# Kernel optimization log

Hardware: AMD Instinct MI355X
Metric: run time of the kernel (lower is better)

## Reference

```python
import jax, jax.numpy as jnp
import numpy as np

H = 128  # hidden_dim


def gcn_conv(x, src, dst, n, W, b):
    """PyG GCNConv: add self-loops, symmetric norm, gather-transform-scatter."""
    h = x @ W  # [n, H]
    loop = jnp.arange(n, dtype=src.dtype)
    s = jnp.concatenate([src, loop])
    d = jnp.concatenate([dst, loop])
    deg = jax.ops.segment_sum(jnp.ones(s.shape[0], h.dtype), d, num_segments=n)
    dinv = jnp.where(deg > 0, jax.lax.rsqrt(deg), 0.0)
    norm = dinv[s] * dinv[d]  # [E+n]
    msg = h[s] * norm[:, None]
    out = jax.ops.segment_sum(msg, d, num_segments=n)
    return out + b


def encode(x, edge_index, batch, num_graphs, params):
    src, dst = edge_index[0], edge_index[1]
    n = x.shape[0]
    for (W, b) in params:
        x = jax.nn.relu(gcn_conv(x, src, dst, n, W, b))
    sums = jax.ops.segment_sum(x, batch, num_segments=num_graphs)
    cnts = jax.ops.segment_sum(jnp.ones((n, 1), x.dtype), batch, num_segments=num_graphs)
    return sums / jnp.maximum(cnts, 1.0)  # global_mean_pool -> [B, H]


def setup_inputs() -> dict:
    key = jax.random.key(0)
    ks = jax.random.split(key, 32)
    B, C = 32, 5
    Nd, Ed = 1280, 5120
    Np, Ep = 12800, 204800
    f32 = jnp.float32

    def lin(k, fan_in, fan_out):
        k1, k2 = jax.random.split(k)
        lim = 1.0 / np.sqrt(fan_in)
        W = jax.random.uniform(k1, (fan_in, fan_out), f32, -lim, lim)
        b = jax.random.uniform(k2, (fan_out,), f32, -lim, lim)
        return W, b

    Wd0, bd0 = lin(ks[0], 78, H)
    Wd1, bd1 = lin(ks[1], H, H)
    Wd2, bd2 = lin(ks[2], H, H)
    Wp0, bp0 = lin(ks[3], 1280, H)
    Wp1, bp1 = lin(ks[4], H, H)
    Wp2, bp2 = lin(ks[5], H, H)
    Wq, bq = lin(ks[6], H, H)
    Wk, bk = lin(ks[7], H, H)
    Wv, bv = lin(ks[8], H, H)
    W1, b1 = lin(ks[9], 2 * H, H)
    W2, b2 = lin(ks[10], H, 1)

    drug_x = jax.random.normal(ks[11], (Nd, 78), f32)
    prot_x = jax.random.normal(ks[12], (C, Np, 1280), f32)
    drug_edge_index = jax.random.randint(ks[13], (2, Ed), 0, Nd, jnp.int32)
    prot_edge_index = jax.random.randint(ks[14], (C, 2, Ep), 0, Np, jnp.int32)
    # equal-sized graphs per batch element -> every segment non-empty
    drug_batch = (jnp.arange(Nd, dtype=jnp.int32) * B) // Nd
    prot_batch = (jnp.arange(Np, dtype=jnp.int32) * B) // Np

    return dict(drug_x=drug_x, prot_x=prot_x,
                Wd0=Wd0, bd0=bd0, Wd1=Wd1, bd1=bd1, Wd2=Wd2, bd2=bd2,
                Wp0=Wp0, bp0=bp0, Wp1=Wp1, bp1=bp1, Wp2=Wp2, bp2=bp2,
                Wq=Wq, bq=bq, Wk=Wk, bk=bk, Wv=Wv, bv=bv,
                W1=W1, b1=b1, W2=W2, b2=b2,
                drug_edge_index=drug_edge_index, prot_edge_index=prot_edge_index,
                drug_batch=drug_batch, prot_batch=prot_batch, num_graphs=B)


def reference(drug_x, prot_x, Wd0, bd0, Wd1, bd1, Wd2, bd2,
              Wp0, bp0, Wp1, bp1, Wp2, bp2,
              Wq, bq, Wk, bk, Wv, bv, W1, b1, W2, b2,
              drug_edge_index, prot_edge_index, drug_batch, prot_batch, num_graphs):
    drug_params = [(Wd0, bd0), (Wd1, bd1), (Wd2, bd2)]
    prot_params = [(Wp0, bp0), (Wp1, bp1), (Wp2, bp2)]

    drug_emb = encode(drug_x, drug_edge_index, drug_batch, num_graphs, drug_params)  # [B,H]

    # vmap over conformations -> [C, B, H]
    conf = jax.vmap(lambda x, ei: encode(x, ei, prot_batch, num_graphs, prot_params))(
        prot_x, prot_edge_index)
    conf = jnp.transpose(conf, (1, 0, 2))  # [B, C, H]

    # drug-conditioned cross-attention over conformations
    q = drug_emb @ Wq + bq                      # [B,H]
    keys = conf @ Wk + bk                       # [B,C,H]
    vals = conf @ Wv + bv                       # [B,C,H]
    scores = jnp.einsum('bh,bch->bc', q, keys) / jnp.sqrt(jnp.asarray(H, q.dtype))
    attn = jax.nn.softmax(scores, axis=1)       # [B,C]
    protein_emb = jnp.einsum('bc,bch->bh', attn, vals)

    combined = jnp.concatenate([drug_emb, protein_emb], axis=1)  # [B,2H]
    hidden = jax.nn.relu(combined @ W1 + b1)    # dropout is identity in eval mode
    logits = (hidden @ W2 + b2)[:, 0]           # [B]
    return logits, attn
```

## Files before the change

### kernel.cpp

```cpp
#include <hip/hip_runtime.h>

#define H     128
#define BGR   32
#define NCONF 5
#define ND    1280
#define FD    78
#define ED    5120
#define NP    12800
#define FP    1280
#define EP    204800
#define MAXD  64

#define PROT_GEMM_BLKS 500
#define DRUG_GEMM1_BLKS 20
#define DRUG_GEMM_BLKS 10
#define PLACE_BLKS 4020
#define PROT_MP_BLKS 16000
#define DRUG_MP_BLKS 320

typedef unsigned short u16;
typedef unsigned int   u32;
typedef __attribute__((ext_vector_type(8))) short bf16x8;
typedef __attribute__((ext_vector_type(4))) unsigned int u32x4;
typedef __attribute__((ext_vector_type(4))) unsigned short u16x4;
typedef __attribute__((ext_vector_type(8))) unsigned short u16x8;
typedef __attribute__((ext_vector_type(4))) float f32x4;

__device__ __forceinline__ u16 f2bf(float x) {
  u32 u = __float_as_uint(x);
  u32 r = (u + 0x7FFFu + ((u >> 16) & 1u)) >> 16;
  return (u16)r;
}
__device__ __forceinline__ float bf2f(u16 h) {
  return __uint_as_float(((u32)h) << 16);
}

__device__ __forceinline__ void gload16(const void* gsrc, void* lds) {
  __builtin_amdgcn_global_load_lds(
      (const __attribute__((address_space(1))) unsigned int*)gsrc,
      (__attribute__((address_space(3))) unsigned int*)lds, 16, 0, 0);
}

__device__ __forceinline__ void cvt8(float4 p, float4 q, bf16x8& hi, bf16x8& lo) {
  float f[8] = {p.x, p.y, p.z, p.w, q.x, q.y, q.z, q.w};
  u32x4 h, l;
  #pragma unroll
  for (int j = 0; j < 4; ++j) {
    u32 u0 = __float_as_uint(f[2 * j]);
    u32 u1 = __float_as_uint(f[2 * j + 1]);
    u32 h0 = u0 & 0xFFFF0000u;
    u32 h1 = u1 & 0xFFFF0000u;
    h[j] = (h0 >> 16) | h1;
    float l0 = f[2 * j]     - __uint_as_float(h0);
    float l1 = f[2 * j + 1] - __uint_as_float(h1);
    l[j] = (__float_as_uint(l0) >> 16) | (__float_as_uint(l1) & 0xFFFF0000u);
  }
  union { u32x4 u; bf16x8 b; } ch, cl;
  ch.u = h; cl.u = l;
  hi = ch.b; lo = cl.b;
}

__device__ __forceinline__ void splitW_chunk(
    const float* __restrict__ W, u16* __restrict__ wsW, int K, int g)
{
  int step = g >> 10;
  int r = g & 1023;
  int col = r >> 3, q = r & 7;
  int u = q ^ (col & 7);
  int kc = (u & 3) * 8;
  bool lo = u >= 4;
  int k0 = step * 32 + kc;
  u16x8 o;
  #pragma unroll
  for (int j = 0; j < 8; ++j) {
    float x = W[(size_t)(k0 + j) * 128 + col];
    u16 h = f2bf(x);
    o[j] = lo ? f2bf(x - bf2f(h)) : h;
  }
  *(u16x8*)(wsW + (size_t)g * 8) = o;
}

__global__ __launch_bounds__(256) void splitW_all_k(
    const float* __restrict__ Wp0, const float* __restrict__ Wp1,
    const float* __restrict__ Wp2, const float* __restrict__ Wd1,
    const float* __restrict__ Wd2,
    u16* __restrict__ o0, u16* __restrict__ o1, u16* __restrict__ o2,
    u16* __restrict__ o3, u16* __restrict__ o4)
{
  int g = blockIdx.x * 256 + threadIdx.x;
  if      (g < 40960) splitW_chunk(Wp0, o0, FP, g);
  else if (g < 45056) splitW_chunk(Wp1, o1, H, g - 40960);
  else if (g < 49152) splitW_chunk(Wp2, o2, H, g - 45056);
  else if (g < 53248) splitW_chunk(Wd1, o3, H, g - 49152);
  else if (g < 57344) splitW_chunk(Wd2, o4, H, g - 53248);
}

__device__ __forceinline__ void gemm_pipe_body(
    char* smemRaw, const float* __restrict__ A, const u16* __restrict__ wsW,
    u16* __restrict__ Cout, int K, int blk)
{
  u16* Wlds = (u16*)smemRaw;
  const int t = threadIdx.x;
  const int wid = t >> 6, lane = t & 63;
  const int lane15 = lane & 15, lq = lane >> 4;
  const int m0 = blk * 128;
  const int NT = K >> 5;

  const float* Ar0 = A + (size_t)(m0 + wid * 32 + lane15) * K + lq * 8;
  const float* Ar1 = Ar0 + (size_t)16 * K;
  const u16* sbase = wsW + (size_t)(wid * 4) * 512 + (size_t)lane * 8;

  f32x4 acc[2][8];
  #pragma unroll
  for (int i = 0; i < 2; ++i)
    #pragma unroll
    for (int j = 0; j < 8; ++j)
      acc[i][j] = (f32x4){0.f, 0.f, 0.f, 0.f};

  #define STAGE_W(step, buf) do {                                   \
    const u16* s_ = sbase + (size_t)(step) * 8192;                  \
    u16* d_ = &Wlds[(buf) * 8192 + wid * 2048];                     \
    gload16(s_,        d_);                                         \
    gload16(s_ + 512,  d_ + 512);                                   \
    gload16(s_ + 1024, d_ + 1024);                                  \
    gload16(s_ + 1536, d_ + 1536);                                  \
  } while (0)

  STAGE_W(0, 0);
  asm volatile("" ::: "memory");
  float4 xa0 = *(const float4*)(Ar0);
  float4 xa1 = *(const float4*)(Ar0 + 4);
  float4 xb0 = *(const float4*)(Ar1);
  float4 xb1 = *(const float4*)(Ar1 + 4);
  asm volatile("" ::: "memory");
  float4 ya0 = *(const float4*)(Ar0 + 32);
  float4 ya1 = *(const float4*)(Ar0 + 36);
  float4 yb0 = *(const float4*)(Ar1 + 32);
  float4 yb1 = *(const float4*)(Ar1 + 36);

  #define BODY(T, RA0, RA1, RB0, RB1) do {                                    \
    if ((T) < NT - 1) asm volatile("s_waitcnt vmcnt(4)\ns_barrier" ::: "memory"); \
    else              asm volatile("s_waitcnt vmcnt(0)\ns_barrier"  ::: "memory"); \
    if ((T) + 1 < NT) { STAGE_W((T) + 1, ((T) + 1) & 1); }                    \
    asm volatile("" ::: "memory");                                            \
    bf16x8 ah0, al0, ah1, al1;                                                \
    cvt8(RA0, RA1, ah0, al0);                                                 \
    cvt8(RB0, RB1, ah1, al1);                                                 \
    if ((T) + 2 < NT) {                                                       \
      const float* p0_ = Ar0 + (size_t)((T) + 2) * 32;                        \
      const float* p1_ = Ar1 + (size_t)((T) + 2) * 32;                        \
      RA0 = *(const float4*)(p0_); RA1 = *(const float4*)(p0_ + 4);           \
      RB0 = *(const float4*)(p1_); RB1 = *(const float4*)(p1_ + 4);           \
    }                                                                         \
    const char* base_ = (const char*)&Wlds[((T) & 1) * 8192];                 \
    _Pragma("unroll")                                                         \
    for (int cb = 0; cb < 8; ++cb) {                                          \
      int col_ = cb * 16 + lane15;                                            \
      const char* cbp_ = base_ + col_ * 128;                                  \
      int sw_ = (col_ & 7) << 4;                                              \
      bf16x8 bh_ = *(const bf16x8*)(cbp_ + ((lq << 4) ^ sw_));                \
      bf16x8 bl_ = *(const bf16x8*)(cbp_ + (((lq | 4) << 4) ^ sw_));          \
      acc[0][cb] = __builtin_amdgcn_mfma_f32_16x16x32_bf16(ah0, bh_, acc[0][cb], 0, 0, 0); \
      acc[0][cb] = __builtin_amdgcn_mfma_f32_16x16x32_bf16(al0, bh_, acc[0][cb], 0, 0, 0); \
      acc[0][cb] = __builtin_amdgcn_mfma_f32_16x16x32_bf16(ah0, bl_, acc[0][cb], 0, 0, 0); \
      acc[1][cb] = __builtin_amdgcn_mfma_f32_16x16x32_bf16(ah1, bh_, acc[1][cb], 0, 0, 0); \
      acc[1][cb] = __builtin_amdgcn_mfma_f32_16x16x32_bf16(al1, bh_, acc[1][cb], 0, 0, 0); \
      acc[1][cb] = __builtin_amdgcn_mfma_f32_16x16x32_bf16(ah1, bl_, acc[1][cb], 0, 0, 0); \
    }                                                                         \
  } while (0)

  for (int tt = 0; tt < NT; tt += 2) {
    BODY(tt,     xa0, xa1, xb0, xb1);
    BODY(tt + 1, ya0, ya1, yb0, yb1);
  }
  #undef BODY
  #undef STAGE_W

  #pragma unroll
  for (int rb = 0; rb < 2; ++rb) {
    #pragma unroll
    for (int j = 0; j < 4; ++j) {
      int row = m0 + wid * 32 + rb * 16 + lq * 4 + j;
      u16* Crow = Cout + (size_t)row * 128 + lane15;
      #pragma unroll
      for (int cb = 0; cb < 8; ++cb)
        Crow[cb * 16] = f2bf(acc[rb][cb][j]);
    }
  }
}

__device__ __forceinline__ void gemm_f32_body(
    char* smemRaw, const float* __restrict__ A, const float* __restrict__ W,
    u16* __restrict__ Cout, int K, int blk)
{
  float* As = (float*)smemRaw;
  float* Bs = (float*)(smemRaw + 16 * 64 * 4);
  const int t = threadIdx.x;
  const int m0 = blk * 64;
  const int colg = (t & 31) * 4;
  const int rowg = (t >> 5) * 8;
  const int rA = t >> 2;
  const int cA = (t & 3) * 4;
  const int rB = t >> 4;
  const int cB = (t & 15) * 4;

  float acc[8][4] = {};

  for (int k0 = 0; k0 < K; k0 += 16) {
    __syncthreads();
    #pragma unroll
    for (int j = 0; j < 4; ++j) {
      int kk = k0 + cA + j;
      As[(cA + j) * 64 + rA] = (kk < K) ? A[(size_t)(m0 + rA) * K + kk] : 0.0f;
    }
    {
      int kk = k0 + rB;
      if (kk < K) {
        *(float4*)&Bs[rB * 128 + cB]      = *(const float4*)(W + (size_t)kk * 128 + cB);
        *(float4*)&Bs[rB * 128 + cB + 64] = *(const float4*)(W + (size_t)kk * 128 + cB + 64);
      } else {
        *(float4*)&Bs[rB * 128 + cB]      = make_float4(0.f, 0.f, 0.f, 0.f);
        *(float4*)&Bs[rB * 128 + cB + 64] = make_float4(0.f, 0.f, 0.f, 0.f);
      }
    }
    __syncthreads();
    #pragma unroll
    for (int k = 0; k < 16; ++k) {
      float4 b  = *(const float4*)&Bs[k * 128 + colg];
      float4 a0 = *(const float4*)&As[k * 64 + rowg];
      float4 a1 = *(const float4*)&As[k * 64 + rowg + 4];
      const float av[8] = {a0.x, a0.y, a0.z, a0.w, a1.x, a1.y, a1.z, a1.w};
      #pragma unroll
      for (int i = 0; i < 8; ++i) {
        acc[i][0] += av[i] * b.x;
        acc[i][1] += av[i] * b.y;
        acc[i][2] += av[i] * b.z;
        acc[i][3] += av[i] * b.w;
      }
    }
  }
  #pragma unroll
  for (int i = 0; i < 8; ++i) {
    u16x4 o;
    o[0] = f2bf(acc[i][0]); o[1] = f2bf(acc[i][1]);
    o[2] = f2bf(acc[i][2]); o[3] = f2bf(acc[i][3]);
    *(u16x4*)(Cout + (size_t)(m0 + rowg + i) * 128 + colg) = o;
  }
}

__global__ __launch_bounds__(256, 4) void stage1_place_k(
    const float* __restrict__ pA, const u16* __restrict__ pW, u16* __restrict__ pC,
    const float* __restrict__ dA, const float* __restrict__ dW, u16* __restrict__ dC,
    const int* __restrict__ prot_ei, const int* __restrict__ drug_ei,
    int* __restrict__ deg_p, u16* __restrict__ slot_p,
    int* __restrict__ deg_d, u16* __restrict__ slot_d)
{
  __shared__ __align__(16) char smem[2 * 16384];
  int b = blockIdx.x;
  if (b < PROT_GEMM_BLKS) {
    gemm_pipe_body(smem, pA, pW, pC, FP, b);
    return;
  }
  b -= PROT_GEMM_BLKS;
  if (b < DRUG_GEMM1_BLKS) {
    gemm_f32_body(smem, dA, dW, dC, FD, b);
    return;
  }
  b -= DRUG_GEMM1_BLKS;
  int idx = b * 256 + threadIdx.x;
  if (idx < NCONF * EP) {
    int c = idx / EP, e = idx - c * EP;
    const int* eic = prot_ei + (size_t)c * 2 * EP;
    int s = eic[e], d = eic[EP + e];
    int node = c * NP + d;
    int pos = atomicAdd(&deg_p[node], 1);
    if (pos < MAXD) slot_p[(size_t)node * MAXD + pos] = (u16)s;
  } else {
    idx -= NCONF * EP;
    if (idx < ED) {
      int s = drug_ei[idx], d = drug_ei[ED + idx];
      int pos = atomicAdd(&deg_d[d], 1);
      if (pos < MAXD) slot_d[(size_t)d * MAXD + pos] = (u16)s;
    }
  }
}

__global__ __launch_bounds__(256, 4) void stage23_gemm_k(
    const float* __restrict__ pA, const u16* __restrict__ pW, u16* __restrict__ pC,
    const float* __restrict__ dA, const u16* __restrict__ dW, u16* __restrict__ dC)
{
  __shared__ __align__(16) char smem[2 * 16384];
  if (blockIdx.x < PROT_GEMM_BLKS)
    gemm_pipe_body(smem, pA, pW, pC, H, blockIdx.x);
  else
    gemm_pipe_body(smem, dA, dW, dC, H, blockIdx.x - PROT_GEMM_BLKS);
}

__device__ __forceinline__ void mp_body(
    const u16* __restrict__ h, float* __restrict__ xout,
    const int* __restrict__ deg, const u16* __restrict__ slots,
    const float* __restrict__ bias, int wid, int nPer)
{
  int lane = threadIdx.x & 63;
  int c = wid / nPer;
  const int* dg = deg + (size_t)c * nPer;
  int v = wid - c * nPer;
  const u32* hc = (const u32*)(h + (size_t)c * nPer * H);
  const u16* sl = slots + (size_t)wid * MAXD;
  int degv = dg[v];
  float dv = rsqrtf((float)degv + 1.0f);
  u32 us = ((const u32*)h)[(size_t)wid * 64 + lane];
  float a0x = __uint_as_float(us << 16) * dv;
  float a0y = __uint_as_float(us & 0xFFFF0000u) * dv;
  float a1x = 0.f, a1y = 0.f;
  int n = degv < MAXD ? degv : MAXD;
  int i = 0;
  for (; i + 4 <= n; i += 4) {
    int s0 = sl[i], s1 = sl[i + 1], s2 = sl[i + 2], s3 = sl[i + 3];
    float d0 = rsqrtf((float)dg[s0] + 1.0f);
    float d1 = rsqrtf((float)dg[s1] + 1.0f);
    float d2 = rsqrtf((float)dg[s2] + 1.0f);
    float d3 = rsqrtf((float)dg[s3] + 1.0f);
    u32 u0 = hc[(size_t)s0 * 64 + lane];
    u32 u1 = hc[(size_t)s1 * 64 + lane];
    u32 u2 = hc[(size_t)s2 * 64 + lane];
    u32 u3 = hc[(size_t)s3 * 64 + lane];
    a0x += __uint_as_float(u0 << 16) * d0;
    a0y += __uint_as_float(u0 & 0xFFFF0000u) * d0;
    a1x += __uint_as_float(u1 << 16) * d1;
    a1y += __uint_as_float(u1 & 0xFFFF0000u) * d1;
    a0x += __uint_as_float(u2 << 16) * d2;
    a0y += __uint_as_float(u2 & 0xFFFF0000u) * d2;
    a1x += __uint_as_float(u3 << 16) * d3;
    a1y += __uint_as_float(u3 & 0xFFFF0000u) * d3;
  }
  for (; i < n; ++i) {
    int s0 = sl[i];
    float d0 = rsqrtf((float)dg[s0] + 1.0f);
    u32 u0 = hc[(size_t)s0 * 64 + lane];
    a0x += __uint_as_float(u0 << 16) * d0;
    a0y += __uint_as_float(u0 & 0xFFFF0000u) * d0;
  }
  int col = lane * 2;
  float ox = fmaxf((a0x + a1x) * dv + bias[col],     0.0f);
  float oy = fmaxf((a0y + a1y) * dv + bias[col + 1], 0.0f);
  ((float2*)(xout + (size_t)wid * H))[lane] = make_float2(ox, oy);
}

__global__ __launch_bounds__(256) void mp_all_k(
    const u16* __restrict__ hp, float* __restrict__ xp,
    const int* __restrict__ degp, const u16* __restrict__ slotp,
    const float* __restrict__ biasp,
    const u16* __restrict__ hd, float* __restrict__ xd,
    const int* __restrict__ degd, const u16* __restrict__ slotd,
    const float* __restrict__ biasd)
{
  int blk = blockIdx.x;
  int wv = threadIdx.x >> 6;
  if (blk < PROT_MP_BLKS) {
    mp_body(hp, xp, degp, slotp, biasp, blk * 4 + wv, NP);
  } else {
    mp_body(hd, xd, degd, slotd, biasd, (blk - PROT_MP_BLKS) * 4 + wv, ND);
  }
}

__device__ __forceinline__ void pool_body(
    const float* __restrict__ x, float* __restrict__ out, int blk, int npg)
{
  __shared__ float part[4][128];
  const int col = threadIdx.x & 127;
  const int rp  = threadIdx.x >> 7;
  size_t row0 = (size_t)blk * npg;
  float acc = 0.0f;
  for (int i = rp; i < npg; i += 4)
    acc += x[(row0 + i) * H + col];
  part[rp][col] = acc;
  __syncthreads();
  if (rp == 0)
    out[(size_t)blk * H + col] =
        (part[0][col] + part[1][col] + part[2][col] + part[3][col]) / (float)npg;
}

__global__ __launch_bounds__(512) void pool_all_k(
    const float* __restrict__ xd, float* __restrict__ outd,
    const float* __restrict__ xp, float* __restrict__ outp)
{
  if (blockIdx.x < BGR) pool_body(xd, outd, blockIdx.x, ND / BGR);
  else                  pool_body(xp, outp, blockIdx.x - BGR, NP / BGR);
}

__global__ __launch_bounds__(128) void attn_mlp_k(
    const float* __restrict__ drug_emb, const float* __restrict__ conf_pool,
    const float* __restrict__ Wq, const float* __restrict__ bq,
    const float* __restrict__ Wk, const float* __restrict__ bk,
    const float* __restrict__ Wv, const float* __restrict__ bv,
    const float* __restrict__ W1, const float* __restrict__ b1,
    const float* __restrict__ W2, const float* __restrict__ b2,
    float* __restrict__ out)
{
  const int b = blockIdx.x;
  const int hcol = threadIdx.x;
  __shared__ float de[H], pc[H], vals_s[NCONF][H], red[H], sc[NCONF], peS[H];

  de[hcol] = drug_emb[(size_t)b * H + hcol];
  __syncthreads();

  float qv = bq[hcol];
  for (int k = 0; k < H; ++k) qv += de[k] * Wq[k * H + hcol];

  for (int c = 0; c < NCONF; ++c) {
    __syncthreads();
    pc[hcol] = conf_pool[((size_t)c * BGR + b) * H + hcol];
    __syncthreads();
    float kk = bk[hcol], vv = bv[hcol];
    for (int k = 0; k < H; ++k) {
      float p = pc[k];
      kk += p * Wk[k * H + hcol];
      vv += p * Wv[k * H + hcol];
    }
    vals_s[c][hcol] = vv;
    red[hcol] = qv * kk;
    __syncthreads();
    for (int s = 64; s > 0; s >>= 1) {
      if (hcol < s) red[hcol] += red[hcol + s];
      __syncthreads();
    }
    if (hcol == 0) sc[c] = red[0] * 0.08838834764831845f;
  }
  __syncthreads();

  float m = sc[0];
  for (int c = 1; c < NCONF; ++c) m = fmaxf(m, sc[c]);
  float ex[NCONF], sum = 0.0f;
  for (int c = 0; c < NCONF; ++c) { ex[c] = expf(sc[c] - m); sum += ex[c]; }
  float inv = 1.0f / sum;
  if (hcol < NCONF) out[BGR + b * NCONF + hcol] = ex[hcol] * inv;

  float pe = 0.0f;
  for (int c = 0; c < NCONF; ++c) pe += (ex[c] * inv) * vals_s[c][hcol];
  peS[hcol] = pe;
  __syncthreads();

  float hid = b1[hcol];
  for (int k = 0; k < H; ++k) hid += de[k]  * W1[k * H + hcol];
  for (int k = 0; k < H; ++k) hid += peS[k] * W1[(H + k) * H + hcol];
  hid = fmaxf(hid, 0.0f);

  red[hcol] = hid * W2[hcol];
  __syncthreads();
  for (int s = 64; s > 0; s >>= 1) {
    if (hcol < s) red[hcol] += red[hcol + s];
    __syncthreads();
  }
  if (hcol == 0) out[b] = red[0] + b2[0];
}

extern "C" void kernel_launch(void* const* d_in, const int* in_sizes, int n_in,
                              void* d_out, int out_size, void* d_ws, size_t ws_size,
                              hipStream_t stream)
{
  const float* drug_x  = (const float*)d_in[0];
  const float* prot_x  = (const float*)d_in[1];
  const float* Wd0 = (const float*)d_in[2];  const float* bd0 = (const float*)d_in[3];
  const float* Wd1 = (const float*)d_in[4];  const float* bd1 = (const float*)d_in[5];
  const float* Wd2 = (const float*)d_in[6];  const float* bd2 = (const float*)d_in[7];
  const float* Wp0 = (const float*)d_in[8];  const float* bp0 = (const float*)d_in[9];
  const float* Wp1 = (const float*)d_in[10]; const float* bp1 = (const float*)d_in[11];
  const float* Wp2 = (const float*)d_in[12]; const float* bp2 = (const float*)d_in[13];
  const float* Wq  = (const float*)d_in[14]; const float* bq  = (const float*)d_in[15];
  const float* Wk  = (const float*)d_in[16]; const float* bk  = (const float*)d_in[17];
  const float* Wv  = (const float*)d_in[18]; const float* bv  = (const float*)d_in[19];
  const float* W1  = (const float*)d_in[20]; const float* b1  = (const float*)d_in[21];
  const float* W2  = (const float*)d_in[22]; const float* b2  = (const float*)d_in[23];
  const int* drug_ei = (const int*)d_in[24];
  const int* prot_ei = (const int*)d_in[25];
  float* out = (float*)d_out;

  char* base = (char*)d_ws;
  size_t off = 0;
  auto alloc = [&](size_t bytes) -> char* {
    char* p = base + off;
    off = (off + bytes + 255) & ~(size_t)255;
    return p;
  };
  int*   deg_p   = (int*)  alloc((size_t)NCONF * NP * 4);
  int*   deg_d   = (int*)  alloc((size_t)ND * 4);
  const size_t ctrBytes = (size_t)NCONF * NP * 4 + (size_t)ND * 4;

  u16*   slot_p  = (u16*)  alloc((size_t)NCONF * NP * MAXD * 2);
  u16*   slot_d  = (u16*)  alloc((size_t)ND * MAXD * 2);
  u16*   bufHp   = (u16*)  alloc((size_t)NCONF * NP * H * 2);
  float* bufXp   = (float*)alloc((size_t)NCONF * NP * H * 4);
  u16*   bufHd   = (u16*)  alloc((size_t)ND * H * 2);
  float* bufXd   = (float*)alloc((size_t)ND * H * 4);
  float* drugemb = (float*)alloc((size_t)BGR * H * 4);
  float* confp   = (float*)alloc((size_t)NCONF * BGR * H * 4);
  u16* Wp0ws = (u16*)alloc((size_t)FP * 512);
  u16* Wp1ws = (u16*)alloc((size_t)H * 512);
  u16* Wp2ws = (u16*)alloc((size_t)H * 512);
  u16* Wd1ws = (u16*)alloc((size_t)H * 512);
  u16* Wd2ws = (u16*)alloc((size_t)H * 512);

  hipMemsetAsync(deg_p, 0, ctrBytes, stream);

  splitW_all_k<<<224, 256, 0, stream>>>(Wp0, Wp1, Wp2, Wd1, Wd2,
                                        Wp0ws, Wp1ws, Wp2ws, Wd1ws, Wd2ws);

  stage1_place_k<<<PROT_GEMM_BLKS + DRUG_GEMM1_BLKS + PLACE_BLKS, 256, 0, stream>>>(
      prot_x, Wp0ws, bufHp, drug_x, Wd0, bufHd,
      prot_ei, drug_ei, deg_p, slot_p, deg_d, slot_d);

  mp_all_k<<<PROT_MP_BLKS + DRUG_MP_BLKS, 256, 0, stream>>>(
      bufHp, bufXp, deg_p, slot_p, bp0,
      bufHd, bufXd, deg_d, slot_d, bd0);
  stage23_gemm_k<<<PROT_GEMM_BLKS + DRUG_GEMM_BLKS, 256, 0, stream>>>(
      bufXp, Wp1ws, bufHp, bufXd, Wd1ws, bufHd);
  mp_all_k<<<PROT_MP_BLKS + DRUG_MP_BLKS, 256, 0, stream>>>(
      bufHp, bufXp, deg_p, slot_p, bp1,
      bufHd, bufXd, deg_d, slot_d, bd1);
  stage23_gemm_k<<<PROT_GEMM_BLKS + DRUG_GEMM_BLKS, 256, 0, stream>>>(
      bufXp, Wp2ws, bufHp, bufXd, Wd2ws, bufHd);
  mp_all_k<<<PROT_MP_BLKS + DRUG_MP_BLKS, 256, 0, stream>>>(
      bufHp, bufXp, deg_p, slot_p, bp2,
      bufHd, bufXd, deg_d, slot_d, bd2);

  pool_all_k<<<BGR + NCONF * BGR, 512, 0, stream>>>(bufXd, drugemb, bufXp, confp);

  attn_mlp_k<<<BGR, 128, 0, stream>>>(drugemb, confp, Wq, bq, Wk, bk, Wv, bv,
                                      W1, b1, W2, b2, out);
}
```

Measured before the change: 410.9 us.

## Store layer activations in bf16 and feed GEMM with bf16 A directly

The message-passing output buffers change from fp32 to bf16, which halves their write traffic, the A-operand reads in the layer 2/3 GEMMs and the pool reads. A new GEMM body loads bf16 A rows directly into MFMA operands instead of converting fp32. The degree-counter memset is folded into the weight-split kernel, removing one API call. In exchange, the activations lose precision: the old path split each value into hi and lo bf16 parts, and now there is a single bf16 rounding, which may affect accuracy.

```diff
diff --git a/kernel.cpp b/kernel.cpp
--- a/kernel.cpp
+++ b/kernel.cpp
@@ -85,9 +85,14 @@
     const float* __restrict__ Wp2, const float* __restrict__ Wd1,
     const float* __restrict__ Wd2,
     u16* __restrict__ o0, u16* __restrict__ o1, u16* __restrict__ o2,
-    u16* __restrict__ o3, u16* __restrict__ o4)
+    u16* __restrict__ o3, u16* __restrict__ o4,
+    int* __restrict__ deg_p, int* __restrict__ deg_d)
 {
   int g = blockIdx.x * 256 + threadIdx.x;
+  for (int i = g; i < NCONF * NP + ND; i += 224 * 256) {
+    if (i < NCONF * NP) deg_p[i] = 0;
+    else                deg_d[i - NCONF * NP] = 0;
+  }
   if      (g < 40960) splitW_chunk(Wp0, o0, FP, g);
   else if (g < 45056) splitW_chunk(Wp1, o1, H, g - 40960);
   else if (g < 49152) splitW_chunk(Wp2, o2, H, g - 45056);
@@ -189,6 +194,92 @@
   }
 }
 
+__device__ __forceinline__ void gemm_pipe_bf16A_body(
+    char* smemRaw, const u16* __restrict__ A, const u16* __restrict__ wsW,
+    u16* __restrict__ Cout, int K, int blk)
+{
+  u16* Wlds = (u16*)smemRaw;
+  const int t = threadIdx.x;
+  const int wid = t >> 6, lane = t & 63;
+  const int lane15 = lane & 15, lq = lane >> 4;
+  const int m0 = blk * 128;
+  const int NT = K >> 5;
+
+  const u16* Ar0 = A + (size_t)(m0 + wid * 32 + lane15) * K + lq * 8;
+  const u16* Ar1 = Ar0 + (size_t)16 * K;
+  const u16* sbase = wsW + (size_t)(wid * 4) * 512 + (size_t)lane * 8;
+
+  f32x4 acc[2][8];
+  #pragma unroll
+  for (int i = 0; i < 2; ++i)
+    #pragma unroll
+    for (int j = 0; j < 8; ++j)
+      acc[i][j] = (f32x4){0.f, 0.f, 0.f, 0.f};
+
+  #define STAGE_W(step, buf) do {                                   \
+    const u16* s_ = sbase + (size_t)(step) * 8192;                  \
+    u16* d_ = &Wlds[(buf) * 8192 + wid * 2048];                     \
+    gload16(s_,        d_);                                         \
+    gload16(s_ + 512,  d_ + 512);                                   \
+    gload16(s_ + 1024, d_ + 1024);                                  \
+    gload16(s_ + 1536, d_ + 1536);                                  \
+  } while (0)
+
+  STAGE_W(0, 0);
+  asm volatile("" ::: "memory");
+  u16x8 xa = *(const u16x8*)(Ar0);
+  u16x8 xb = *(const u16x8*)(Ar1);
+  asm volatile("" ::: "memory");
+  u16x8 ya = *(const u16x8*)(Ar0 + 32);
+  u16x8 yb = *(const u16x8*)(Ar1 + 32);
+
+  #define BODYB(T, RA, RB) do {                                               \
+    if ((T) < NT - 1) asm volatile("s_waitcnt vmcnt(2)\ns_barrier" ::: "memory"); \
+    else              asm volatile("s_waitcnt vmcnt(0)\ns_barrier"  ::: "memory"); \
+    if ((T) + 1 < NT) { STAGE_W((T) + 1, ((T) + 1) & 1); }                    \
+    asm volatile("" ::: "memory");                                            \
+    union { u16x8 u; bf16x8 b; } ca_, cb2_;                                   \
+    ca_.u = RA; cb2_.u = RB;                                                  \
+    bf16x8 a0 = ca_.b, a1 = cb2_.b;                                           \
+    if ((T) + 2 < NT) {                                                       \
+      RA = *(const u16x8*)(Ar0 + (size_t)((T) + 2) * 32);                     \
+      RB = *(const u16x8*)(Ar1 + (size_t)((T) + 2) * 32);                     \
+    }                                                                         \
+    const char* base_ = (const char*)&Wlds[((T) & 1) * 8192];                 \
+    _Pragma("unroll")                                                         \
+    for (int cb = 0; cb < 8; ++cb) {                                          \
+      int col_ = cb * 16 + lane15;                                            \
+      const char* cbp_ = base_ + col_ * 128;                                  \
+      int sw_ = (col_ & 7) << 4;                                              \
+      bf16x8 bh_ = *(const bf16x8*)(cbp_ + ((lq << 4) ^ sw_));                \
+      bf16x8 bl_ = *(const bf16x8*)(cbp_ + (((lq | 4) << 4) ^ sw_));          \
+      acc[0][cb] = __builtin_amdgcn_mfma_f32_16x16x32_bf16(a0, bh_, acc[0][cb], 0, 0, 0); \
+      acc[0][cb] = __builtin_amdgcn_mfma_f32_16x16x32_bf16(a0, bl_, acc[0][cb], 0, 0, 0); \
+      acc[1][cb] = __builtin_amdgcn_mfma_f32_16x16x32_bf16(a1, bh_, acc[1][cb], 0, 0, 0); \
+      acc[1][cb] = __builtin_amdgcn_mfma_f32_16x16x32_bf16(a1, bl_, acc[1][cb], 0, 0, 0); \
+    }                                                                         \
+  } while (0)
+
+  for (int tt = 0; tt < NT; tt += 2) {
+    BODYB(tt,     xa, xb);
+    BODYB(tt + 1, ya, yb);
+  }
+  #undef BODYB
+  #undef STAGE_W
+
+  #pragma unroll
+  for (int rb = 0; rb < 2; ++rb) {
+    #pragma unroll
+    for (int j = 0; j < 4; ++j) {
+      int row = m0 + wid * 32 + rb * 16 + lq * 4 + j;
+      u16* Crow = Cout + (size_t)row * 128 + lane15;
+      #pragma unroll
+      for (int cb = 0; cb < 8; ++cb)
+        Crow[cb * 16] = f2bf(acc[rb][cb][j]);
+    }
+  }
+}
+
 __device__ __forceinline__ void gemm_f32_body(
     char* smemRaw, const float* __restrict__ A, const float* __restrict__ W,
     u16* __restrict__ Cout, int K, int blk)
@@ -286,18 +377,18 @@
 }
 
 __global__ __launch_bounds__(256, 4) void stage23_gemm_k(
-    const float* __restrict__ pA, const u16* __restrict__ pW, u16* __restrict__ pC,
-    const float* __restrict__ dA, const u16* __restrict__ dW, u16* __restrict__ dC)
+    const u16* __restrict__ pA, const u16* __restrict__ pW, u16* __restrict__ pC,
+    const u16* __restrict__ dA, const u16* __restrict__ dW, u16* __restrict__ dC)
 {
   __shared__ __align__(16) char smem[2 * 16384];
   if (blockIdx.x < PROT_GEMM_BLKS)
-    gemm_pipe_body(smem, pA, pW, pC, H, blockIdx.x);
+    gemm_pipe_bf16A_body(smem, pA, pW, pC, H, blockIdx.x);
   else
-    gemm_pipe_body(smem, dA, dW, dC, H, blockIdx.x - PROT_GEMM_BLKS);
+    gemm_pipe_bf16A_body(smem, dA, dW, dC, H, blockIdx.x - PROT_GEMM_BLKS);
 }
 
 __device__ __forceinline__ void mp_body(
-    const u16* __restrict__ h, float* __restrict__ xout,
+    const u16* __restrict__ h, u16* __restrict__ xout,
     const int* __restrict__ deg, const u16* __restrict__ slots,
     const float* __restrict__ bias, int wid, int nPer)
 {
@@ -344,14 +435,15 @@
   int col = lane * 2;
   float ox = fmaxf((a0x + a1x) * dv + bias[col],     0.0f);
   float oy = fmaxf((a0y + a1y) * dv + bias[col + 1], 0.0f);
-  ((float2*)(xout + (size_t)wid * H))[lane] = make_float2(ox, oy);
+  u32 ow = (u32)f2bf(ox) | ((u32)f2bf(oy) << 16);
+  ((u32*)xout)[(size_t)wid * 64 + lane] = ow;
 }
 
 __global__ __launch_bounds__(256) void mp_all_k(
-    const u16* __restrict__ hp, float* __restrict__ xp,
+    const u16* __restrict__ hp, u16* __restrict__ xp,
     const int* __restrict__ degp, const u16* __restrict__ slotp,
     const float* __restrict__ biasp,
-    const u16* __restrict__ hd, float* __restrict__ xd,
+    const u16* __restrict__ hd, u16* __restrict__ xd,
     const int* __restrict__ degd, const u16* __restrict__ slotd,
     const float* __restrict__ biasd)
 {
@@ -365,7 +457,7 @@
 }
 
 __device__ __forceinline__ void pool_body(
-    const float* __restrict__ x, float* __restrict__ out, int blk, int npg)
+    const u16* __restrict__ x, float* __restrict__ out, int blk, int npg)
 {
   __shared__ float part[4][128];
   const int col = threadIdx.x & 127;
@@ -373,7 +465,7 @@
   size_t row0 = (size_t)blk * npg;
   float acc = 0.0f;
   for (int i = rp; i < npg; i += 4)
-    acc += x[(row0 + i) * H + col];
+    acc += bf2f(x[(row0 + i) * H + col]);
   part[rp][col] = acc;
   __syncthreads();
   if (rp == 0)
@@ -382,8 +474,8 @@
 }
 
 __global__ __launch_bounds__(512) void pool_all_k(
-    const float* __restrict__ xd, float* __restrict__ outd,
-    const float* __restrict__ xp, float* __restrict__ outp)
+    const u16* __restrict__ xd, float* __restrict__ outd,
+    const u16* __restrict__ xp, float* __restrict__ outp)
 {
   if (blockIdx.x < BGR) pool_body(xd, outd, blockIdx.x, ND / BGR);
   else                  pool_body(xp, outp, blockIdx.x - BGR, NP / BGR);
@@ -485,14 +577,12 @@
   };
   int*   deg_p   = (int*)  alloc((size_t)NCONF * NP * 4);
   int*   deg_d   = (int*)  alloc((size_t)ND * 4);
-  const size_t ctrBytes = (size_t)NCONF * NP * 4 + (size_t)ND * 4;
-
   u16*   slot_p  = (u16*)  alloc((size_t)NCONF * NP * MAXD * 2);
   u16*   slot_d  = (u16*)  alloc((size_t)ND * MAXD * 2);
   u16*   bufHp   = (u16*)  alloc((size_t)NCONF * NP * H * 2);
-  float* bufXp   = (float*)alloc((size_t)NCONF * NP * H * 4);
+  u16*   bufXp   = (u16*)  alloc((size_t)NCONF * NP * H * 2);
   u16*   bufHd   = (u16*)  alloc((size_t)ND * H * 2);
-  float* bufXd   = (float*)alloc((size_t)ND * H * 4);
+  u16*   bufXd   = (u16*)  alloc((size_t)ND * H * 2);
   float* drugemb = (float*)alloc((size_t)BGR * H * 4);
   float* confp   = (float*)alloc((size_t)NCONF * BGR * H * 4);
   u16* Wp0ws = (u16*)alloc((size_t)FP * 512);
@@ -501,10 +591,9 @@
   u16* Wd1ws = (u16*)alloc((size_t)H * 512);
   u16* Wd2ws = (u16*)alloc((size_t)H * 512);
 
-  hipMemsetAsync(deg_p, 0, ctrBytes, stream);
-
   splitW_all_k<<<224, 256, 0, stream>>>(Wp0, Wp1, Wp2, Wd1, Wd2,
-                                        Wp0ws, Wp1ws, Wp2ws, Wd1ws, Wd2ws);
+                                        Wp0ws, Wp1ws, Wp2ws, Wd1ws, Wd2ws,
+                                        deg_p, deg_d);
 
   stage1_place_k<<<PROT_GEMM_BLKS + DRUG_GEMM1_BLKS + PLACE_BLKS, 256, 0, stream>>>(
       prot_x, Wp0ws, bufHp, drug_x, Wd0, bufHd,
```

Measured after the change: 391.4 us. -4.7%, faster.
